# Kernel optimization log

Hardware: AMD Instinct MI355X
Metric: run time of the kernel (lower is better)

Reference implementation:

```python
import jax, jax.numpy as jnp
import numpy as np

B, C, H, W = 2, 96, 40, 40
DIN, N, R, K = 192, 16, 6, 4  # d_inner, d_state, dt_rank, k_group


def silu(x):
    return x * jax.nn.sigmoid(x)


def dwconv3x3(x, w, b):
    # depthwise 3x3, SAME padding; w: (DIN,1,3,3)
    y = jax.lax.conv_general_dilated(x, w, (1, 1), [(1, 1), (1, 1)],
                                     feature_group_count=x.shape[1])
    return y + b[None, :, None, None]


def cross_scan(x):
    # (B,C,H,W) -> (B,4,C,L): row-major, col-major, and their reverses
    b, c, h, w = x.shape
    x0 = x.reshape(b, c, h * w)
    x1 = x.transpose(0, 1, 3, 2).reshape(b, c, h * w)
    return jnp.stack([x0, x1, x0[..., ::-1], x1[..., ::-1]], axis=1)


def cross_merge(y, h, w):
    # (B,4,C,H,W) -> (B,C,L)
    b, k, c = y.shape[0], y.shape[1], y.shape[2]
    y = y.reshape(b, k, c, h * w)
    y = y[:, :2] + y[:, 2:][..., ::-1]
    y1 = y[:, 1].reshape(b, c, w, h).transpose(0, 1, 3, 2).reshape(b, c, h * w)
    return y[:, 0] + y1


def selective_scan(u, dt, A, Bm, Cm, Dv, dbias):
    # u, dt: (B,K,DIN,L); A: (K*DIN,N); Bm, Cm: (B,K,N,L); Dv: (K*DIN,); dbias: (K*DIN,)
    b, k, d, l = u.shape
    n = A.shape[1]
    A4 = A.reshape(k, d, n)
    dt = jax.nn.softplus(dt + dbias.reshape(1, k, d, 1))
    # discretize: dA = exp(dt*A), dBu = dt*B*u  -> shapes (B,K,D,L,N)
    dA = jnp.exp(dt[..., None] * A4[None, :, :, None, :])
    dBu = dt[..., None] * Bm.transpose(0, 1, 3, 2)[:, :, None, :, :] * u[..., None]

    def combine(c1, c2):
        a1, b1 = c1
        a2, b2 = c2
        return a1 * a2, a2 * b1 + b2

    _, h = jax.lax.associative_scan(combine, (dA, dBu), axis=3)  # h: (B,K,D,L,N)
    y = jnp.einsum('bkdln,bknl->bkdl', h, Cm)
    return y + Dv.reshape(1, k, d, 1) * u


def ln2d(x, g, b):
    # LayerNorm over channel dim (channel_first LayerNorm2d)
    mu = x.mean(axis=1, keepdims=True)
    var = jnp.mean((x - mu) ** 2, axis=1, keepdims=True)
    xn = (x - mu) / jnp.sqrt(var + 1e-5)
    return xn * g[None, :, None, None] + b[None, :, None, None]


def setup_inputs():
    key = jax.random.key(0)
    ks = jax.random.split(key, 24)

    def rn(k, shape, s=0.02):
        return jax.random.normal(k, shape, dtype=jnp.float32) * s

    A_log = jnp.tile(jnp.log(jnp.arange(1, N + 1, dtype=jnp.float32))[None, :], (K * DIN, 1))
    return {
        'x_rgb': jax.random.normal(ks[0], (B, C, H, W), jnp.float32),
        'x_e': jax.random.normal(ks[1], (B, C, H, W), jnp.float32),
        'in_proj_w': rn(ks[2], (DIN, C)),
        'in_proj_mx_w': rn(ks[3], (DIN, C)),
        'conv_w': rn(ks[4], (DIN, 1, 3, 3), 0.1),
        'conv_b': jnp.zeros((DIN,), jnp.float32),
        'xproj1_w': rn(ks[5], (K, R + 2 * N, DIN)),
        'xproj2_w': rn(ks[6], (K, R + 2 * N, DIN)),
        'dtproj1_w': rn(ks[7], (K, DIN, R), 0.1),
        'dtproj1_b': rn(ks[8], (K, DIN), 0.1) - 4.0,
        'dtproj2_w': rn(ks[9], (K, DIN, R), 0.1),
        'dtproj2_b': rn(ks[10], (K, DIN), 0.1) - 4.0,
        'A_log_1': A_log,
        'A_log_2': A_log,
        'D_1': jnp.ones((K * DIN,), jnp.float32),
        'D_2': jnp.ones((K * DIN,), jnp.float32),
        'norm1_g': jnp.ones((DIN,), jnp.float32),
        'norm1_b': jnp.zeros((DIN,), jnp.float32),
        'norm2_g': jnp.ones((DIN,), jnp.float32),
        'norm2_b': jnp.zeros((DIN,), jnp.float32),
        'fc1_w1': rn(ks[11], (DIN // 16, DIN), 0.05),
        'fc1_w2': rn(ks[12], (DIN, DIN // 16), 0.05),
        'fc2_w1': rn(ks[13], (DIN // 16, DIN), 0.05),
        'fc2_w2': rn(ks[14], (DIN, DIN // 16), 0.05),
        'out_proj_w': rn(ks[15], (C, 2 * DIN)),
    }


def reference(x_rgb, x_e, in_proj_w, in_proj_mx_w, conv_w, conv_b, xproj1_w, xproj2_w,
              dtproj1_w, dtproj1_b, dtproj2_w, dtproj2_b, A_log_1, A_log_2, D_1, D_2,
              norm1_g, norm1_b, norm2_g, norm2_b, fc1_w1, fc1_w2, fc2_w1, fc2_w2, out_proj_w):
    # in_proj (1x1 conv style Linear2d)
    xr = jnp.einsum('oc,bchw->bohw', in_proj_w, x_rgb)
    xe = jnp.einsum('oc,bchw->bohw', in_proj_mx_w, x_e)
    # shared depthwise conv + SiLU
    xr = silu(dwconv3x3(xr, conv_w, conv_b))
    xe = silu(dwconv3x3(xe, conv_w, conv_b))
    b, d, h, w = xr.shape

    xs_r = cross_scan(xr)  # (B,K,DIN,L)
    xs_e = cross_scan(xe)

    def proj(xs, xp_w, dt_w):
        t = jnp.einsum('bkdl,kcd->bkcl', xs, xp_w)  # grouped 1x1 conv1d
        dts, Bm, Cm = jnp.split(t, [R, R + N], axis=2)
        dts = jnp.einsum('bkrl,kdr->bkdl', dts, dt_w)
        return dts, Bm, Cm

    d_r, B_r, C_r = proj(xs_r, xproj1_w, dtproj1_w)
    d_e, B_e, C_e = proj(xs_e, xproj2_w, dtproj2_w)

    # cross attention: rgb scan consumes C and D of the other modality
    y_r = selective_scan(xs_r, d_r, -jnp.exp(A_log_1), B_r, C_e, D_2, dtproj1_b.reshape(-1))
    y_e = selective_scan(xs_e, d_e, -jnp.exp(A_log_2), B_e, C_r, D_1, dtproj2_b.reshape(-1))

    y_r = cross_merge(y_r.reshape(b, K, d, h, w), h, w).reshape(b, d, h, w)
    y_e = cross_merge(y_e.reshape(b, K, d, h, w), h, w).reshape(b, d, h, w)
    y_r = ln2d(y_r, norm1_g, norm1_b)
    y_e = ln2d(y_e, norm2_g, norm2_b)

    # cross squeeze-excitation
    sq_r = xr.mean(axis=(2, 3))
    sq_e = xe.mean(axis=(2, 3))
    exc_r = jax.nn.sigmoid(silu(sq_r @ fc1_w1.T) @ fc1_w2.T)
    exc_e = jax.nn.sigmoid(silu(sq_e @ fc2_w1.T) @ fc2_w2.T)
    y_r = y_r * exc_e[:, :, None, None]
    y_e = y_e * exc_r[:, :, None, None]

    y = jnp.concatenate([y_r, y_e], axis=1)  # (B, 2*DIN, H, W)
    return jnp.einsum('oc,bchw->bohw', out_proj_w, y)
```

## Files before the change

### kernel.cpp

```cpp
#include <hip/hip_runtime.h>
#include <math.h>

#define BN   2
#define CIN  96
#define HH   40
#define WW   40
#define LL   1600
#define DIN  192
#define NS   16
#define RR   6
#define KK   4
#define CH   25

__device__ __forceinline__ float sigmoidf_(float x){ return 1.0f/(1.0f+expf(-x)); }
__device__ __forceinline__ float softplus_fast(float x){
  return x > 20.0f ? x : __logf(1.0f + __expf(x));
}

__device__ __forceinline__ void pow_tree(float R, float* p){
  float R2 = R * R;
  float R4 = R2 * R2;
  float R8 = R4 * R4;
  p[0]  = R;        p[1]  = R2;       p[2]  = R2 * R;   p[3]  = R4;
  p[4]  = R4 * R;   p[5]  = R4 * R2;  p[6]  = R4 * p[2];p[7]  = R8;
  p[8]  = R8 * R;   p[9]  = R8 * R2;  p[10] = R8 * p[2];p[11] = R8 * R4;
  p[12] = R8 * p[4];p[13] = R8 * p[5];p[14] = R8 * p[6];p[15] = R8 * R8;
}

__global__ void k_inproj(const float* __restrict__ x_rgb, const float* __restrict__ x_e,
                         const float* __restrict__ w_rgb, const float* __restrict__ w_e,
                         float* __restrict__ xproj){
  __shared__ float xin[16][100];
  int l0 = blockIdx.x * 16;
  int mb = blockIdx.y;
  int m = mb / BN, b = mb % BN;
  const float* xsrc = (m == 0 ? x_rgb : x_e) + (size_t)b * CIN * LL;
  const float* w    = (m == 0 ? w_rgb : w_e);
  for (int idx = threadIdx.x; idx < CIN * 16; idx += 256){
    int c = idx >> 4, px = idx & 15;
    xin[px][c] = xsrc[c * LL + l0 + px];
  }
  __syncthreads();
  int px = threadIdx.x & 15;
  int o0 = (threadIdx.x >> 4) * 12;
  float acc[12];
  #pragma unroll
  for (int i = 0; i < 12; ++i) acc[i] = 0.f;
  const float4* xv = reinterpret_cast<const float4*>(xin[px]);
  for (int cc = 0; cc < CIN / 4; ++cc){
    float4 x4 = xv[cc];
    #pragma unroll
    for (int i = 0; i < 12; ++i){
      float4 w4 = *reinterpret_cast<const float4*>(w + (o0 + i) * CIN + cc * 4);
      acc[i] += w4.x * x4.x + w4.y * x4.y + w4.z * x4.z + w4.w * x4.w;
    }
  }
  #pragma unroll
  for (int i = 0; i < 12; ++i)
    xproj[((size_t)mb * DIN + o0 + i) * LL + l0 + px] = acc[i];
}

__global__ void k_conv(const float* __restrict__ xproj, const float* __restrict__ conv_w,
                       const float* __restrict__ conv_b, float* __restrict__ x_act,
                       float* __restrict__ x_actT, float* __restrict__ u_chA,
                       float* __restrict__ u_chT, float* __restrict__ sq){
  __shared__ float pl[LL];
  __shared__ float sact[LL + HH];
  __shared__ float red[4];
  int d  = blockIdx.x;
  int mb = blockIdx.y;
  const float* src = xproj + ((size_t)mb * DIN + d) * LL;
  for (int p = threadIdx.x; p < LL; p += blockDim.x) pl[p] = src[p];
  __syncthreads();
  float cw[9];
  #pragma unroll
  for (int j = 0; j < 9; ++j) cw[j] = conv_w[d * 9 + j];
  float bias = conv_b[d];
  float* dst = x_act + ((size_t)mb * DIN + d) * LL;
  float lsum = 0.f;
  for (int p = threadIdx.x; p < LL; p += blockDim.x){
    int py = p / WW, px = p % WW;
    float acc = bias;
    #pragma unroll
    for (int dy = -1; dy <= 1; ++dy){
      int yy = py + dy;
      if (yy < 0 || yy >= HH) continue;
      #pragma unroll
      for (int dx = -1; dx <= 1; ++dx){
        int xx = px + dx;
        if (xx < 0 || xx >= WW) continue;
        acc += cw[(dy + 1) * 3 + (dx + 1)] * pl[yy * WW + xx];
      }
    }
    float s = acc * sigmoidf_(acc);
    dst[p] = s;
    sact[p + p / WW] = s;
    lsum += s;
  }
  #pragma unroll
  for (int off = 32; off; off >>= 1) lsum += __shfl_down(lsum, off);
  if ((threadIdx.x & 63) == 0) red[threadIdx.x >> 6] = lsum;
  __syncthreads();
  if (threadIdx.x == 0)
    sq[mb * DIN + d] = (red[0] + red[1] + red[2] + red[3]) * (1.0f / LL);
  size_t po = ((size_t)mb * DIN + d) * LL;
  float* dstT = x_actT + po;
  float* uA   = u_chA + po;
  float* uT   = u_chT + po;
  for (int q = threadIdx.x; q < LL; q += blockDim.x){
    int lt = (q % WW) * WW + q / WW;
    dstT[q] = sact[lt + lt / WW];
    int l = (q & 63) * CH + (q >> 6);
    uA[q] = sact[l + l / WW];
    int pt = (l % WW) * WW + l / WW;
    uT[q] = sact[pt + pt / WW];
  }
}

__global__ void k_xproj(const float* __restrict__ x_act, const float* __restrict__ x_actT,
                        const float* __restrict__ xp1, const float* __restrict__ xp2,
                        float* __restrict__ tdt_ch, float* __restrict__ B_ch,
                        float* __restrict__ C_ch){
  int l0 = blockIdx.x * 64;
  int k  = blockIdx.y;
  int mb = blockIdx.z; int m = mb / BN;
  const float* xw = (m == 0 ? xp1 : xp2) + k * 38 * DIN;
  const float* xa = ((k & 1) ? x_actT : x_act) + (size_t)mb * DIN * LL;
  bool rev = (k >= 2);
  int ll = threadIdx.x & 63;
  int g  = threadIdx.x >> 6;
  int c0 = g * 10;
  int l  = l0 + ll; if (rev) l = LL - 1 - l;
  const float* xcol = xa + l;
  float acc[10];
  #pragma unroll
  for (int i = 0; i < 10; ++i) acc[i] = 0.f;
  if (g < 3){
    for (int dd = 0; dd < DIN; ++dd){
      float xv = xcol[(size_t)dd * LL];
      #pragma unroll
      for (int i = 0; i < 10; ++i) acc[i] += xw[(c0 + i) * DIN + dd] * xv;
    }
  } else {
    for (int dd = 0; dd < DIN; ++dd){
      float xv = xcol[(size_t)dd * LL];
      #pragma unroll
      for (int i = 0; i < 8; ++i) acc[i] += xw[(c0 + i) * DIN + dd] * xv;
    }
  }
  int mbk = mb * KK + k;
  int lq = l0 + ll;
  int q = (lq % CH) * 64 + lq / CH;
  int nc = (g < 3) ? 10 : 8;
  for (int i = 0; i < nc; ++i){
    int c = c0 + i;
    float v = acc[i];
    if (c < RR){
      tdt_ch[((size_t)mbk * RR + c) * LL + q] = v;
    } else if (c < RR + NS){
      int n = c - RR;
      B_ch[(((size_t)mbk * 4 + (n >> 2)) * LL + q) * 4 + (n & 3)] = v;
    } else {
      int n = c - RR - NS;
      C_ch[(((size_t)mbk * 4 + (n >> 2)) * LL + q) * 4 + (n & 3)] = v;
    }
  }
}

__global__ void __launch_bounds__(256, 4) k_scan(
    const float* __restrict__ u_chA, const float* __restrict__ u_chT,
    const float* __restrict__ tdt_all, const float* __restrict__ B_ch,
    const float* __restrict__ C_ch,
    const float* __restrict__ Alog1, const float* __restrict__ Alog2,
    const float* __restrict__ D1, const float* __restrict__ D2,
    const float* __restrict__ dtw1, const float* __restrict__ dtb1,
    const float* __restrict__ dtw2, const float* __restrict__ dtb2,
    float* __restrict__ y_px){
  __shared__ _Float16 ysth[4][LL];
  __shared__ float dt_lds[4][LL];
  int wv   = threadIdx.x >> 6;
  int lane = threadIdx.x & 63;
  int chain = blockIdx.x * 4 + wv;
  int d   = chain % DIN;
  int mbk = chain / DIN;
  int k   = mbk % KK;
  int mb  = mbk / KK;
  int m = mb / BN, b = mb % BN;
  int kd = k * DIN + d;
  bool rev = (k >= 2);

  const float* Alog = (m == 0 ? Alog1 : Alog2) + kd * NS;
  float An[NS];
  bool fastA = true;
  #pragma unroll
  for (int n = 0; n < NS; ++n){
    An[n] = -__expf(Alog[n]);
    fastA = fastA && (fabsf(An[n] + (float)(n + 1)) <= 1e-4f * (float)(n + 1));
  }
  float Dv = (m == 0 ? D2 : D1)[kd];
  const float* dtw = (m == 0 ? dtw1 : dtw2) + kd * RR;
  float w0 = dtw[0], w1 = dtw[1], w2 = dtw[2], w3 = dtw[3], w4 = dtw[4], w5 = dtw[5];
  float dbias = (m == 0 ? dtb1 : dtb2)[kd];

  const float* t0 = tdt_all + (size_t)mbk * RR * LL;
  for (int s = 0; s < CH; ++s){
    int q = s * 64 + lane;
    float dtpre = w0 * t0[q] + w1 * t0[LL + q] + w2 * t0[2 * LL + q]
                + w3 * t0[3 * LL + q] + w4 * t0[4 * LL + q] + w5 * t0[5 * LL + q] + dbias;
    dt_lds[wv][q] = softplus_fast(dtpre);
  }

  const float4* B0 = reinterpret_cast<const float4*>(B_ch) + (size_t)mbk * 4 * LL;
  int mbk_o = ((1 - m) * BN + b) * KK + k;
  const float4* C0 = reinterpret_cast<const float4*>(C_ch) + (size_t)mbk_o * 4 * LL;
  const float* urow = ((k & 1) ? u_chT : u_chA) + ((size_t)mb * DIN + d) * LL;

  float h[NS];
  #pragma unroll
  for (int n = 0; n < NS; ++n) h[n] = 0.f;
  float Sdt = 0.f;

  if (fastA){
    float4 bP[4], cP[4]; float uP, dtP;
    {
      int q0 = lane;
      dtP = dt_lds[wv][q0];
      uP  = urow[rev ? (LL - 1 - q0) : q0];
      bP[0]=B0[q0]; bP[1]=B0[LL+q0]; bP[2]=B0[2*LL+q0]; bP[3]=B0[3*LL+q0];
      cP[0]=C0[q0]; cP[1]=C0[LL+q0]; cP[2]=C0[2*LL+q0]; cP[3]=C0[3*LL+q0];
    }
    #pragma unroll 5
    for (int s = 0; s < CH; ++s){
      float dt = dtP, u = uP;
      float4 b0=bP[0], b1=bP[1], b2=bP[2], b3=bP[3];
      float4 c0=cP[0], c1=cP[1], c2=cP[2], c3=cP[3];
      if (s + 1 < CH){
        int q1 = (s + 1) * 64 + lane;
        dtP = dt_lds[wv][q1];
        uP  = urow[rev ? (LL - 1 - q1) : q1];
        bP[0]=B0[q1]; bP[1]=B0[LL+q1]; bP[2]=B0[2*LL+q1]; bP[3]=B0[3*LL+q1];
        cP[0]=C0[q1]; cP[1]=C0[LL+q1]; cP[2]=C0[2*LL+q1]; cP[3]=C0[3*LL+q1];
      }
      Sdt += dt;
      float du = dt * u;
      float Bv[NS] = {b0.x,b0.y,b0.z,b0.w, b1.x,b1.y,b1.z,b1.w,
                      b2.x,b2.y,b2.z,b2.w, b3.x,b3.y,b3.z,b3.w};
      float Cv[NS] = {c0.x,c0.y,c0.z,c0.w, c1.x,c1.y,c1.z,c1.w,
                      c2.x,c2.y,c2.z,c2.w, c3.x,c3.y,c3.z,c3.w};
      float p[NS];
      pow_tree(__expf(-dt), p);
      float y0 = Dv * u, y1 = 0.f, y2 = 0.f, y3 = 0.f;
      #pragma unroll
      for (int n = 0; n < NS; ++n){
        h[n] = p[n] * h[n] + du * Bv[n];
        float t = h[n] * Cv[n];
        if      ((n & 3) == 0) y0 += t;
        else if ((n & 3) == 1) y1 += t;
        else if ((n & 3) == 2) y2 += t;
        else                   y3 += t;
      }
      ysth[wv][lane * CH + s] = (_Float16)((y0 + y1) + (y2 + y3));
    }
  } else {
    #pragma unroll 5
    for (int s = 0; s < CH; ++s){
      int q = s * 64 + lane;
      float dt = dt_lds[wv][q];
      Sdt += dt;
      float u  = urow[rev ? (LL - 1 - q) : q];
      float du = dt * u;
      float4 b0 = B0[q], b1 = B0[LL + q], b2 = B0[2 * LL + q], b3 = B0[3 * LL + q];
      float4 c0 = C0[q], c1 = C0[LL + q], c2 = C0[2 * LL + q], c3 = C0[3 * LL + q];
      float Bv[NS] = {b0.x,b0.y,b0.z,b0.w, b1.x,b1.y,b1.z,b1.w,
                      b2.x,b2.y,b2.z,b2.w, b3.x,b3.y,b3.z,b3.w};
      float Cv[NS] = {c0.x,c0.y,c0.z,c0.w, c1.x,c1.y,c1.z,c1.w,
                      c2.x,c2.y,c2.z,c2.w, c3.x,c3.y,c3.z,c3.w};
      float y0 = Dv * u, y1 = 0.f, y2 = 0.f, y3 = 0.f;
      #pragma unroll
      for (int n = 0; n < NS; ++n){
        float dA = __expf(dt * An[n]);
        h[n] = dA * h[n] + du * Bv[n];
        float t = h[n] * Cv[n];
        if      ((n & 3) == 0) y0 += t;
        else if ((n & 3) == 1) y1 += t;
        else if ((n & 3) == 2) y2 += t;
        else                   y3 += t;
      }
      ysth[wv][lane * CH + s] = (_Float16)((y0 + y1) + (y2 + y3));
    }
  }
  float aP[NS];
  if (fastA){
    pow_tree(__expf(-Sdt), aP);
  } else {
    #pragma unroll
    for (int n = 0; n < NS; ++n) aP[n] = __expf(Sdt * An[n]);
  }

  #pragma unroll
  for (int off = 1; off < 64; off <<= 1){
    #pragma unroll
    for (int n = 0; n < NS; ++n){
      float ap = __shfl_up(aP[n], off);
      float bp = __shfl_up(h[n],  off);
      if (lane >= off){
        h[n]  = aP[n] * bp + h[n];
        aP[n] = aP[n] * ap;
      }
    }
  }
  #pragma unroll
  for (int n = 0; n < NS; ++n){
    float v = __shfl_up(h[n], 1);
    h[n] = (lane == 0) ? 0.f : v;
  }

  if (fastA){
    float4 cP[4]; float dtP;
    {
      int q0 = lane;
      dtP = dt_lds[wv][q0];
      cP[0]=C0[q0]; cP[1]=C0[LL+q0]; cP[2]=C0[2*LL+q0]; cP[3]=C0[3*LL+q0];
    }
    float cum = 0.f;
    #pragma unroll 5
    for (int s = 0; s < CH; ++s){
      float dt = dtP;
      float4 c0=cP[0], c1=cP[1], c2=cP[2], c3=cP[3];
      if (s + 1 < CH){
        int q1 = (s + 1) * 64 + lane;
        dtP = dt_lds[wv][q1];
        cP[0]=C0[q1]; cP[1]=C0[LL+q1]; cP[2]=C0[2*LL+q1]; cP[3]=C0[3*LL+q1];
      }
      cum += dt;
      float Rc = __expf(-cum);
      float Cv[NS] = {c0.x,c0.y,c0.z,c0.w, c1.x,c1.y,c1.z,c1.w,
                      c2.x,c2.y,c2.z,c2.w, c3.x,c3.y,c3.z,c3.w};
      float p[NS];
      pow_tree(Rc, p);
      float s0 = 0.f, s1 = 0.f, s2 = 0.f, s3 = 0.f;
      #pragma unroll
      for (int n = 0; n < NS; ++n){
        float t = h[n] * p[n] * Cv[n];
        if      ((n & 3) == 0) s0 += t;
        else if ((n & 3) == 1) s1 += t;
        else if ((n & 3) == 2) s2 += t;
        else                   s3 += t;
      }
      int li = lane * CH + s;
      ysth[wv][li] = (_Float16)((float)ysth[wv][li] + (s0 + s1) + (s2 + s3));
    }
  } else {
    float cum = 0.f;
    #pragma unroll 5
    for (int s = 0; s < CH; ++s){
      int q = s * 64 + lane;
      cum += dt_lds[wv][q];
      float4 c0 = C0[q], c1 = C0[LL + q], c2 = C0[2 * LL + q], c3 = C0[3 * LL + q];
      float Cv[NS] = {c0.x,c0.y,c0.z,c0.w, c1.x,c1.y,c1.z,c1.w,
                      c2.x,c2.y,c2.z,c2.w, c3.x,c3.y,c3.z,c3.w};
      float s0 = 0.f, s1 = 0.f, s2 = 0.f, s3 = 0.f;
      #pragma unroll
      for (int n = 0; n < NS; ++n){
        float t = h[n] * __expf(cum * An[n]) * Cv[n];
        if      ((n & 3) == 0) s0 += t;
        else if ((n & 3) == 1) s1 += t;
        else if ((n & 3) == 2) s2 += t;
        else                   s3 += t;
      }
      int li = lane * CH + s;
      ysth[wv][li] = (_Float16)((float)ysth[wv][li] + (s0 + s1) + (s2 + s3));
    }
  }

  float* yo = y_px + (size_t)chain * LL;
  for (int qq = lane; qq < LL; qq += 64){
    int l;
    if      (k == 0) l = qq;
    else if (k == 1) l = (qq % WW) * WW + qq / WW;
    else if (k == 2) l = LL - 1 - qq;
    else             { int qt = (qq % WW) * WW + qq / WW; l = LL - 1 - qt; }
    yo[qq] = (float)ysth[wv][l];
  }
}

__global__ void __launch_bounds__(256) k_mergeout(
    const float* __restrict__ y_px, const float* __restrict__ sq,
    const float* __restrict__ fc1_w1, const float* __restrict__ fc1_w2,
    const float* __restrict__ fc2_w1, const float* __restrict__ fc2_w2,
    const float* __restrict__ n1g, const float* __restrict__ n1b,
    const float* __restrict__ n2g, const float* __restrict__ n2b,
    const float* __restrict__ wout, float* __restrict__ out){
  __shared__ float acc[2 * DIN][9];
  __shared__ float yt[8][388];
  __shared__ float ps[2][8][16], ps2[2][8][16];
  __shared__ float mu_s[2][8], inv_s[2][8];
  __shared__ float sqs[2][DIN];
  __shared__ float hid[2][12];
  __shared__ float exc_s[2][DIN];
  int p0 = blockIdx.x * 8;
  int b  = blockIdx.y;
  int tid = threadIdx.x;
  for (int idx = tid; idx < 2 * DIN * 8; idx += 256){
    int pp = idx & 7, row = idx >> 3;
    int mm = (row >= DIN), dd = row - mm * DIN;
    const float* yb = y_px + ((size_t)(mm * BN + b) * KK * DIN + dd) * LL + p0 + pp;
    acc[row][pp] = yb[0] + yb[(size_t)DIN * LL]
                 + yb[2 * (size_t)DIN * LL] + yb[3 * (size_t)DIN * LL];
  }
  for (int i = tid; i < 2 * DIN; i += 256){
    int mm = (i >= DIN), dd = i - mm * DIN;
    sqs[mm][dd] = sq[((1 - mm) * BN + b) * DIN + dd];
  }
  __syncthreads();
  if (tid < 24){
    int mm = tid / 12, j = tid - mm * 12;
    const float* w1 = (mm == 1 ? fc1_w1 : fc2_w1);
    float a = 0.f;
    for (int cch = 0; cch < DIN; ++cch) a += w1[j * DIN + cch] * sqs[mm][cch];
    hid[mm][j] = a * sigmoidf_(a);
  }
  {
    int pp = tid & 7, mm = (tid >> 3) & 1, g = tid >> 4;
    float s = 0.f, s2 = 0.f;
    #pragma unroll 4
    for (int j = 0; j < 12; ++j){
      float v = acc[mm * DIN + g * 12 + j][pp];
      s += v; s2 += v * v;
    }
    ps[mm][pp][g] = s; ps2[mm][pp][g] = s2;
  }
  __syncthreads();
  if (tid < 16){
    int mm = tid >> 3, pp = tid & 7;
    float s = 0.f, s2 = 0.f;
    #pragma unroll
    for (int g = 0; g < 16; ++g){ s += ps[mm][pp][g]; s2 += ps2[mm][pp][g]; }
    float mu  = s * (1.0f / DIN);
    float var = s2 * (1.0f / DIN) - mu * mu;
    mu_s[mm][pp] = mu; inv_s[mm][pp] = rsqrtf(var + 1e-5f);
  }
  for (int i = tid; i < 2 * DIN; i += 256){
    int mm = (i >= DIN), dd = i - mm * DIN;
    const float* w2 = (mm == 1 ? fc1_w2 : fc2_w2);
    float e = 0.f;
    #pragma unroll
    for (int j = 0; j < 12; ++j) e += w2[dd * 12 + j] * hid[mm][j];
    exc_s[mm][dd] = sigmoidf_(e);
  }
  __syncthreads();
  for (int idx = tid; idx < 2 * DIN * 8; idx += 256){
    int pp = idx & 7, row = idx >> 3;
    int mm = (row >= DIN), dd = row - mm * DIN;
    float g  = (mm ? n2g : n1g)[dd];
    float bb = (mm ? n2b : n1b)[dd];
    float v = (acc[row][pp] - mu_s[mm][pp]) * inv_s[mm][pp] * g + bb;
    yt[pp][row] = v * exc_s[mm][dd];
  }
  __syncthreads();
  int pp = tid & 7;
  int o0 = (tid >> 3) * 3;
  float a3[3] = {0.f, 0.f, 0.f};
  const float4* yv = reinterpret_cast<const float4*>(yt[pp]);
  for (int cc = 0; cc < 96; ++cc){
    float4 x4 = yv[cc];
    #pragma unroll
    for (int i = 0; i < 3; ++i){
      float4 w4 = *reinterpret_cast<const float4*>(wout + (o0 + i) * 2 * DIN + cc * 4);
      a3[i] += w4.x * x4.x + w4.y * x4.y + w4.z * x4.z + w4.w * x4.w;
    }
  }
  #pragma unroll
  for (int i = 0; i < 3; ++i)
    out[((size_t)b * CIN + o0 + i) * LL + p0 + pp] = a3[i];
}

extern "C" void kernel_launch(void* const* d_in, const int* in_sizes, int n_in,
                              void* d_out, int out_size, void* d_ws, size_t ws_size,
                              hipStream_t stream){
  const float* x_rgb   = (const float*)d_in[0];
  const float* x_e     = (const float*)d_in[1];
  const float* in_w    = (const float*)d_in[2];
  const float* in_mx_w = (const float*)d_in[3];
  const float* conv_w  = (const float*)d_in[4];
  const float* conv_b  = (const float*)d_in[5];
  const float* xp1     = (const float*)d_in[6];
  const float* xp2     = (const float*)d_in[7];
  const float* dtw1    = (const float*)d_in[8];
  const float* dtb1    = (const float*)d_in[9];
  const float* dtw2    = (const float*)d_in[10];
  const float* dtb2    = (const float*)d_in[11];
  const float* Alog1   = (const float*)d_in[12];
  const float* Alog2   = (const float*)d_in[13];
  const float* D1      = (const float*)d_in[14];
  const float* D2      = (const float*)d_in[15];
  const float* n1g     = (const float*)d_in[16];
  const float* n1b     = (const float*)d_in[17];
  const float* n2g     = (const float*)d_in[18];
  const float* n2b     = (const float*)d_in[19];
  const float* fc1_w1  = (const float*)d_in[20];
  const float* fc1_w2  = (const float*)d_in[21];
  const float* fc2_w1  = (const float*)d_in[22];
  const float* fc2_w2  = (const float*)d_in[23];
  const float* wout    = (const float*)d_in[24];

  float* ws = (float*)d_ws;
  float* u_chA   = ws;
  float* u_chT   = ws + 1228800;
  float* x_act   = ws + 2457600;
  float* x_actT  = ws + 3686400;
  float* xproj   = ws + 4915200;
  float* y_px    = ws + 6144000;
  float* B_ch    = ws + 11059200;
  float* C_ch    = ws + 11468800;
  float* tdt_ch  = ws + 11878400;
  float* sq      = ws + 12032000;

  k_inproj  <<<dim3(LL / 16, 2 * BN), 256, 0, stream>>>(x_rgb, x_e, in_w, in_mx_w, xproj);
  k_conv    <<<dim3(DIN, 2 * BN), 256, 0, stream>>>(xproj, conv_w, conv_b,
                                                    x_act, x_actT, u_chA, u_chT, sq);
  k_xproj   <<<dim3(LL / 64, KK, 2 * BN), 256, 0, stream>>>(x_act, x_actT, xp1, xp2,
                                                            tdt_ch, B_ch, C_ch);
  k_scan    <<<768, 256, 0, stream>>>(u_chA, u_chT, tdt_ch, B_ch, C_ch,
                                      Alog1, Alog2, D1, D2,
                                      dtw1, dtb1, dtw2, dtb2, y_px);
  k_mergeout<<<dim3(LL / 8, BN), 256, 0, stream>>>(y_px, sq,
                                                   fc1_w1, fc1_w2, fc2_w1, fc2_w2,
                                                   n1g, n1b, n2g, n2b,
                                                   wout, (float*)d_out);
}
```

Baseline: 168.0 us.

## Store intermediate activations, B/C, and scan outputs in fp16

Converts the intermediate buffers (activated conv output and its transposes, the scan u inputs, the B and C projections, and the per-direction scan outputs) from fp32 to fp16. B and C are repacked as 8-wide half groups so each element is fetched with two float4 loads instead of four. All arithmetic stays in fp32 after unpacking. The aim is to roughly halve global memory traffic across several kernels, at the cost of fp16 rounding error on activations and outputs.

```diff
diff --git a/kernel.cpp b/kernel.cpp
--- a/kernel.cpp
+++ b/kernel.cpp
@@ -12,6 +12,8 @@
 #define KK   4
 #define CH   25
 
+typedef _Float16 h16;
+
 __device__ __forceinline__ float sigmoidf_(float x){ return 1.0f/(1.0f+expf(-x)); }
 __device__ __forceinline__ float softplus_fast(float x){
   return x > 20.0f ? x : __logf(1.0f + __expf(x));
@@ -25,6 +27,12 @@
   p[4]  = R4 * R;   p[5]  = R4 * R2;  p[6]  = R4 * p[2];p[7]  = R8;
   p[8]  = R8 * R;   p[9]  = R8 * R2;  p[10] = R8 * p[2];p[11] = R8 * R4;
   p[12] = R8 * p[4];p[13] = R8 * p[5];p[14] = R8 * p[6];p[15] = R8 * R8;
+}
+
+__device__ __forceinline__ void unpack8(float4 v, float* dst){
+  const h16* hp = reinterpret_cast<const h16*>(&v);
+  #pragma unroll
+  for (int i = 0; i < 8; ++i) dst[i] = (float)hp[i];
 }
 
 __global__ void k_inproj(const float* __restrict__ x_rgb, const float* __restrict__ x_e,
@@ -61,9 +69,9 @@
 }
 
 __global__ void k_conv(const float* __restrict__ xproj, const float* __restrict__ conv_w,
-                       const float* __restrict__ conv_b, float* __restrict__ x_act,
-                       float* __restrict__ x_actT, float* __restrict__ u_chA,
-                       float* __restrict__ u_chT, float* __restrict__ sq){
+                       const float* __restrict__ conv_b, h16* __restrict__ x_act,
+                       h16* __restrict__ x_actT, h16* __restrict__ u_chA,
+                       h16* __restrict__ u_chT, float* __restrict__ sq){
   __shared__ float pl[LL];
   __shared__ float sact[LL + HH];
   __shared__ float red[4];
@@ -76,7 +84,7 @@
   #pragma unroll
   for (int j = 0; j < 9; ++j) cw[j] = conv_w[d * 9 + j];
   float bias = conv_b[d];
-  float* dst = x_act + ((size_t)mb * DIN + d) * LL;
+  h16* dst = x_act + ((size_t)mb * DIN + d) * LL;
   float lsum = 0.f;
   for (int p = threadIdx.x; p < LL; p += blockDim.x){
     int py = p / WW, px = p % WW;
@@ -93,7 +101,7 @@
       }
     }
     float s = acc * sigmoidf_(acc);
-    dst[p] = s;
+    dst[p] = (h16)s;
     sact[p + p / WW] = s;
     lsum += s;
   }
@@ -104,46 +112,46 @@
   if (threadIdx.x == 0)
     sq[mb * DIN + d] = (red[0] + red[1] + red[2] + red[3]) * (1.0f / LL);
   size_t po = ((size_t)mb * DIN + d) * LL;
-  float* dstT = x_actT + po;
-  float* uA   = u_chA + po;
-  float* uT   = u_chT + po;
+  h16* dstT = x_actT + po;
+  h16* uA   = u_chA + po;
+  h16* uT   = u_chT + po;
   for (int q = threadIdx.x; q < LL; q += blockDim.x){
     int lt = (q % WW) * WW + q / WW;
-    dstT[q] = sact[lt + lt / WW];
+    dstT[q] = (h16)sact[lt + lt / WW];
     int l = (q & 63) * CH + (q >> 6);
-    uA[q] = sact[l + l / WW];
+    uA[q] = (h16)sact[l + l / WW];
     int pt = (l % WW) * WW + l / WW;
-    uT[q] = sact[pt + pt / WW];
-  }
-}
-
-__global__ void k_xproj(const float* __restrict__ x_act, const float* __restrict__ x_actT,
+    uT[q] = (h16)sact[pt + pt / WW];
+  }
+}
+
+__global__ void k_xproj(const h16* __restrict__ x_act, const h16* __restrict__ x_actT,
                         const float* __restrict__ xp1, const float* __restrict__ xp2,
-                        float* __restrict__ tdt_ch, float* __restrict__ B_ch,
-                        float* __restrict__ C_ch){
+                        float* __restrict__ tdt_ch, h16* __restrict__ B_ch,
+                        h16* __restrict__ C_ch){
   int l0 = blockIdx.x * 64;
   int k  = blockIdx.y;
   int mb = blockIdx.z; int m = mb / BN;
   const float* xw = (m == 0 ? xp1 : xp2) + k * 38 * DIN;
-  const float* xa = ((k & 1) ? x_actT : x_act) + (size_t)mb * DIN * LL;
+  const h16* xa = ((k & 1) ? x_actT : x_act) + (size_t)mb * DIN * LL;
   bool rev = (k >= 2);
   int ll = threadIdx.x & 63;
   int g  = threadIdx.x >> 6;
   int c0 = g * 10;
   int l  = l0 + ll; if (rev) l = LL - 1 - l;
-  const float* xcol = xa + l;
+  const h16* xcol = xa + l;
   float acc[10];
   #pragma unroll
   for (int i = 0; i < 10; ++i) acc[i] = 0.f;
   if (g < 3){
     for (int dd = 0; dd < DIN; ++dd){
-      float xv = xcol[(size_t)dd * LL];
+      float xv = (float)xcol[(size_t)dd * LL];
       #pragma unroll
       for (int i = 0; i < 10; ++i) acc[i] += xw[(c0 + i) * DIN + dd] * xv;
     }
   } else {
     for (int dd = 0; dd < DIN; ++dd){
-      float xv = xcol[(size_t)dd * LL];
+      float xv = (float)xcol[(size_t)dd * LL];
       #pragma unroll
       for (int i = 0; i < 8; ++i) acc[i] += xw[(c0 + i) * DIN + dd] * xv;
     }
@@ -159,24 +167,24 @@
       tdt_ch[((size_t)mbk * RR + c) * LL + q] = v;
     } else if (c < RR + NS){
       int n = c - RR;
-      B_ch[(((size_t)mbk * 4 + (n >> 2)) * LL + q) * 4 + (n & 3)] = v;
+      B_ch[(((size_t)mbk * 2 + (n >> 3)) * LL + q) * 8 + (n & 7)] = (h16)v;
     } else {
       int n = c - RR - NS;
-      C_ch[(((size_t)mbk * 4 + (n >> 2)) * LL + q) * 4 + (n & 3)] = v;
+      C_ch[(((size_t)mbk * 2 + (n >> 3)) * LL + q) * 8 + (n & 7)] = (h16)v;
     }
   }
 }
 
 __global__ void __launch_bounds__(256, 4) k_scan(
-    const float* __restrict__ u_chA, const float* __restrict__ u_chT,
-    const float* __restrict__ tdt_all, const float* __restrict__ B_ch,
-    const float* __restrict__ C_ch,
+    const h16* __restrict__ u_chA, const h16* __restrict__ u_chT,
+    const float* __restrict__ tdt_all, const h16* __restrict__ B_ch,
+    const h16* __restrict__ C_ch,
     const float* __restrict__ Alog1, const float* __restrict__ Alog2,
     const float* __restrict__ D1, const float* __restrict__ D2,
     const float* __restrict__ dtw1, const float* __restrict__ dtb1,
     const float* __restrict__ dtw2, const float* __restrict__ dtb2,
-    float* __restrict__ y_px){
-  __shared__ _Float16 ysth[4][LL];
+    h16* __restrict__ y_px){
+  __shared__ h16 ysth[4][LL];
   __shared__ float dt_lds[4][LL];
   int wv   = threadIdx.x >> 6;
   int lane = threadIdx.x & 63;
@@ -210,10 +218,10 @@
     dt_lds[wv][q] = softplus_fast(dtpre);
   }
 
-  const float4* B0 = reinterpret_cast<const float4*>(B_ch) + (size_t)mbk * 4 * LL;
+  const float4* B0 = reinterpret_cast<const float4*>(B_ch) + (size_t)mbk * 2 * LL;
   int mbk_o = ((1 - m) * BN + b) * KK + k;
-  const float4* C0 = reinterpret_cast<const float4*>(C_ch) + (size_t)mbk_o * 4 * LL;
-  const float* urow = ((k & 1) ? u_chT : u_chA) + ((size_t)mb * DIN + d) * LL;
+  const float4* C0 = reinterpret_cast<const float4*>(C_ch) + (size_t)mbk_o * 2 * LL;
+  const h16* urow = ((k & 1) ? u_chT : u_chA) + ((size_t)mb * DIN + d) * LL;
 
   float h[NS];
   #pragma unroll
@@ -221,32 +229,30 @@
   float Sdt = 0.f;
 
   if (fastA){
-    float4 bP[4], cP[4]; float uP, dtP;
+    float4 bP0, bP1, cP0, cP1; float uP, dtP;
     {
       int q0 = lane;
       dtP = dt_lds[wv][q0];
-      uP  = urow[rev ? (LL - 1 - q0) : q0];
-      bP[0]=B0[q0]; bP[1]=B0[LL+q0]; bP[2]=B0[2*LL+q0]; bP[3]=B0[3*LL+q0];
-      cP[0]=C0[q0]; cP[1]=C0[LL+q0]; cP[2]=C0[2*LL+q0]; cP[3]=C0[3*LL+q0];
+      uP  = (float)urow[rev ? (LL - 1 - q0) : q0];
+      bP0 = B0[q0]; bP1 = B0[LL + q0];
+      cP0 = C0[q0]; cP1 = C0[LL + q0];
     }
     #pragma unroll 5
     for (int s = 0; s < CH; ++s){
       float dt = dtP, u = uP;
-      float4 b0=bP[0], b1=bP[1], b2=bP[2], b3=bP[3];
-      float4 c0=cP[0], c1=cP[1], c2=cP[2], c3=cP[3];
+      float4 b0 = bP0, b1 = bP1, c0 = cP0, c1 = cP1;
       if (s + 1 < CH){
         int q1 = (s + 1) * 64 + lane;
         dtP = dt_lds[wv][q1];
-        uP  = urow[rev ? (LL - 1 - q1) : q1];
-        bP[0]=B0[q1]; bP[1]=B0[LL+q1]; bP[2]=B0[2*LL+q1]; bP[3]=B0[3*LL+q1];
-        cP[0]=C0[q1]; cP[1]=C0[LL+q1]; cP[2]=C0[2*LL+q1]; cP[3]=C0[3*LL+q1];
+        uP  = (float)urow[rev ? (LL - 1 - q1) : q1];
+        bP0 = B0[q1]; bP1 = B0[LL + q1];
+        cP0 = C0[q1]; cP1 = C0[LL + q1];
       }
       Sdt += dt;
       float du = dt * u;
-      float Bv[NS] = {b0.x,b0.y,b0.z,b0.w, b1.x,b1.y,b1.z,b1.w,
-                      b2.x,b2.y,b2.z,b2.w, b3.x,b3.y,b3.z,b3.w};
-      float Cv[NS] = {c0.x,c0.y,c0.z,c0.w, c1.x,c1.y,c1.z,c1.w,
-                      c2.x,c2.y,c2.z,c2.w, c3.x,c3.y,c3.z,c3.w};
+      float Bv[NS], Cv[NS];
+      unpack8(b0, Bv); unpack8(b1, Bv + 8);
+      unpack8(c0, Cv); unpack8(c1, Cv + 8);
       float p[NS];
       pow_tree(__expf(-dt), p);
       float y0 = Dv * u, y1 = 0.f, y2 = 0.f, y3 = 0.f;
@@ -259,7 +265,7 @@
         else if ((n & 3) == 2) y2 += t;
         else                   y3 += t;
       }
-      ysth[wv][lane * CH + s] = (_Float16)((y0 + y1) + (y2 + y3));
+      ysth[wv][lane * CH + s] = (h16)((y0 + y1) + (y2 + y3));
     }
   } else {
     #pragma unroll 5
@@ -267,14 +273,11 @@
       int q = s * 64 + lane;
       float dt = dt_lds[wv][q];
       Sdt += dt;
-      float u  = urow[rev ? (LL - 1 - q) : q];
+      float u  = (float)urow[rev ? (LL - 1 - q) : q];
       float du = dt * u;
-      float4 b0 = B0[q], b1 = B0[LL + q], b2 = B0[2 * LL + q], b3 = B0[3 * LL + q];
-      float4 c0 = C0[q], c1 = C0[LL + q], c2 = C0[2 * LL + q], c3 = C0[3 * LL + q];
-      float Bv[NS] = {b0.x,b0.y,b0.z,b0.w, b1.x,b1.y,b1.z,b1.w,
-                      b2.x,b2.y,b2.z,b2.w, b3.x,b3.y,b3.z,b3.w};
-      float Cv[NS] = {c0.x,c0.y,c0.z,c0.w, c1.x,c1.y,c1.z,c1.w,
-                      c2.x,c2.y,c2.z,c2.w, c3.x,c3.y,c3.z,c3.w};
+      float Bv[NS], Cv[NS];
+      unpack8(B0[q], Bv); unpack8(B0[LL + q], Bv + 8);
+      unpack8(C0[q], Cv); unpack8(C0[LL + q], Cv + 8);
       float y0 = Dv * u, y1 = 0.f, y2 = 0.f, y3 = 0.f;
       #pragma unroll
       for (int n = 0; n < NS; ++n){
@@ -286,7 +289,7 @@
         else if ((n & 3) == 2) y2 += t;
         else                   y3 += t;
       }
-      ysth[wv][lane * CH + s] = (_Float16)((y0 + y1) + (y2 + y3));
+      ysth[wv][lane * CH + s] = (h16)((y0 + y1) + (y2 + y3));
     }
   }
   float aP[NS];
@@ -316,26 +319,26 @@
   }
 
   if (fastA){
-    float4 cP[4]; float dtP;
+    float4 cP0, cP1; float dtP;
     {
       int q0 = lane;
       dtP = dt_lds[wv][q0];
-      cP[0]=C0[q0]; cP[1]=C0[LL+q0]; cP[2]=C0[2*LL+q0]; cP[3]=C0[3*LL+q0];
+      cP0 = C0[q0]; cP1 = C0[LL + q0];
     }
     float cum = 0.f;
     #pragma unroll 5
     for (int s = 0; s < CH; ++s){
       float dt = dtP;
-      float4 c0=cP[0], c1=cP[1], c2=cP[2], c3=cP[3];
+      float4 c0 = cP0, c1 = cP1;
       if (s + 1 < CH){
         int q1 = (s + 1) * 64 + lane;
         dtP = dt_lds[wv][q1];
-        cP[0]=C0[q1]; cP[1]=C0[LL+q1]; cP[2]=C0[2*LL+q1]; cP[3]=C0[3*LL+q1];
+        cP0 = C0[q1]; cP1 = C0[LL + q1];
       }
       cum += dt;
       float Rc = __expf(-cum);
-      float Cv[NS] = {c0.x,c0.y,c0.z,c0.w, c1.x,c1.y,c1.z,c1.w,
-                      c2.x,c2.y,c2.z,c2.w, c3.x,c3.y,c3.z,c3.w};
+      float Cv[NS];
+      unpack8(c0, Cv); unpack8(c1, Cv + 8);
       float p[NS];
       pow_tree(Rc, p);
       float s0 = 0.f, s1 = 0.f, s2 = 0.f, s3 = 0.f;
@@ -348,7 +351,7 @@
         else                   s3 += t;
       }
       int li = lane * CH + s;
-      ysth[wv][li] = (_Float16)((float)ysth[wv][li] + (s0 + s1) + (s2 + s3));
+      ysth[wv][li] = (h16)((float)ysth[wv][li] + (s0 + s1) + (s2 + s3));
     }
   } else {
     float cum = 0.f;
@@ -356,9 +359,8 @@
     for (int s = 0; s < CH; ++s){
       int q = s * 64 + lane;
       cum += dt_lds[wv][q];
-      float4 c0 = C0[q], c1 = C0[LL + q], c2 = C0[2 * LL + q], c3 = C0[3 * LL + q];
-      float Cv[NS] = {c0.x,c0.y,c0.z,c0.w, c1.x,c1.y,c1.z,c1.w,
-                      c2.x,c2.y,c2.z,c2.w, c3.x,c3.y,c3.z,c3.w};
+      float Cv[NS];
+      unpack8(C0[q], Cv); unpack8(C0[LL + q], Cv + 8);
       float s0 = 0.f, s1 = 0.f, s2 = 0.f, s3 = 0.f;
       #pragma unroll
       for (int n = 0; n < NS; ++n){
@@ -369,23 +371,23 @@
         else                   s3 += t;
       }
       int li = lane * CH + s;
-      ysth[wv][li] = (_Float16)((float)ysth[wv][li] + (s0 + s1) + (s2 + s3));
-    }
-  }
-
-  float* yo = y_px + (size_t)chain * LL;
+      ysth[wv][li] = (h16)((float)ysth[wv][li] + (s0 + s1) + (s2 + s3));
+    }
+  }
+
+  h16* yo = y_px + (size_t)chain * LL;
   for (int qq = lane; qq < LL; qq += 64){
     int l;
     if      (k == 0) l = qq;
     else if (k == 1) l = (qq % WW) * WW + qq / WW;
     else if (k == 2) l = LL - 1 - qq;
     else             { int qt = (qq % WW) * WW + qq / WW; l = LL - 1 - qt; }
-    yo[qq] = (float)ysth[wv][l];
+    yo[qq] = ysth[wv][l];
   }
 }
 
 __global__ void __launch_bounds__(256) k_mergeout(
-    const float* __restrict__ y_px, const float* __restrict__ sq,
+    const h16* __restrict__ y_px, const float* __restrict__ sq,
     const float* __restrict__ fc1_w1, const float* __restrict__ fc1_w2,
     const float* __restrict__ fc2_w1, const float* __restrict__ fc2_w2,
     const float* __restrict__ n1g, const float* __restrict__ n1b,
@@ -404,9 +406,9 @@
   for (int idx = tid; idx < 2 * DIN * 8; idx += 256){
     int pp = idx & 7, row = idx >> 3;
     int mm = (row >= DIN), dd = row - mm * DIN;
-    const float* yb = y_px + ((size_t)(mm * BN + b) * KK * DIN + dd) * LL + p0 + pp;
-    acc[row][pp] = yb[0] + yb[(size_t)DIN * LL]
-                 + yb[2 * (size_t)DIN * LL] + yb[3 * (size_t)DIN * LL];
+    const h16* yb = y_px + ((size_t)(mm * BN + b) * KK * DIN + dd) * LL + p0 + pp;
+    acc[row][pp] = (float)yb[0] + (float)yb[(size_t)DIN * LL]
+                 + (float)yb[2 * (size_t)DIN * LL] + (float)yb[3 * (size_t)DIN * LL];
   }
   for (int i = tid; i < 2 * DIN; i += 256){
     int mm = (i >= DIN), dd = i - mm * DIN;
@@ -505,14 +507,14 @@
   const float* wout    = (const float*)d_in[24];
 
   float* ws = (float*)d_ws;
-  float* u_chA   = ws;
-  float* u_chT   = ws + 1228800;
-  float* x_act   = ws + 2457600;
-  float* x_actT  = ws + 3686400;
+  h16*   u_chA   = (h16*)(ws);
+  h16*   u_chT   = (h16*)(ws + 1228800);
+  h16*   x_act   = (h16*)(ws + 2457600);
+  h16*   x_actT  = (h16*)(ws + 3686400);
   float* xproj   = ws + 4915200;
-  float* y_px    = ws + 6144000;
-  float* B_ch    = ws + 11059200;
-  float* C_ch    = ws + 11468800;
+  h16*   y_px    = (h16*)(ws + 6144000);
+  h16*   B_ch    = (h16*)(ws + 11059200);
+  h16*   C_ch    = (h16*)(ws + 11468800);
   float* tdt_ch  = ws + 11878400;
   float* sq      = ws + 12032000;
 
```

Measured after the change: 156.8 us. -6.6%, faster.
